# Performance work log

Hardware: AMD Instinct MI355X
Metric: run time of the kernel (lower is better)

The kernel has to match this reference:

```python
import jax, jax.numpy as jnp
import numpy as np


def setup_inputs() -> dict:
    key = jax.random.key(0)
    ks = jax.random.split(key, 13)
    B, T, C = 256, 80, 512
    H = 512
    NC = 6625
    S = 25
    s = 0.02
    inp = {
        "inputs": jax.random.normal(ks[0], (B, T, C), jnp.float32),
        "targets": jax.random.randint(ks[1], (B, S), 0, NC),
        "batch_max_length": S,
        "i2h_w": jax.random.normal(ks[2], (H, C), jnp.float32) * s,
        "h2h_w": jax.random.normal(ks[3], (H, H), jnp.float32) * s,
        "h2h_b": jax.random.normal(ks[4], (H,), jnp.float32) * s,
        "score_w": jax.random.normal(ks[5], (1, H), jnp.float32) * s,
        "gru_wih": jax.random.normal(ks[6], (3 * H, C + NC), jnp.float32) * s,
        "gru_whh": jax.random.normal(ks[7], (3 * H, H), jnp.float32) * s,
        "gru_bih": jax.random.normal(ks[8], (3 * H,), jnp.float32) * s,
        "gru_bhh": jax.random.normal(ks[9], (3 * H,), jnp.float32) * s,
        "gen_w": jax.random.normal(ks[10], (NC, H), jnp.float32) * s,
        "gen_b": jax.random.normal(ks[11], (NC,), jnp.float32) * s,
    }
    return inp


def reference(inputs, targets, batch_max_length, i2h_w, h2h_w, h2h_b, score_w,
              gru_wih, gru_whh, gru_bih, gru_bhh, gen_w, gen_b):
    B, T, C = inputs.shape
    H = h2h_w.shape[0]
    NC = gen_w.shape[0]
    S = batch_max_length

    # i2h has no bias; same result every step, hoisted out of the loop
    batch_H_proj = inputs @ i2h_w.T  # [B, T, H]
    # teacher-forcing one-hots for all steps: [S, B, NC]
    onehots = jax.nn.one_hot(targets.T, NC, dtype=inputs.dtype)

    def gru_cell(x, h):
        gi = x @ gru_wih.T + gru_bih  # [B, 3H]
        gh = h @ gru_whh.T + gru_bhh  # [B, 3H]
        i_r, i_z, i_n = jnp.split(gi, 3, axis=1)
        h_r, h_z, h_n = jnp.split(gh, 3, axis=1)
        r = jax.nn.sigmoid(i_r + h_r)
        z = jax.nn.sigmoid(i_z + h_z)
        n = jnp.tanh(i_n + r * h_n)
        return (1.0 - z) * n + z * h

    def step(h, onehot_t):
        prev_proj = h @ h2h_w.T + h2h_b  # [B, H]
        res = jnp.tanh(batch_H_proj + prev_proj[:, None, :])  # [B, T, H]
        e = jnp.einsum('bth,h->bt', res, score_w[0])  # [B, T]
        alpha = jax.nn.softmax(e, axis=1)
        context = jnp.einsum('bt,btc->bc', alpha, inputs)  # [B, C]
        x = jnp.concatenate([context, onehot_t], axis=1)  # [B, C+NC]
        h_new = gru_cell(x, h)
        return h_new, h_new

    h0 = jnp.zeros((B, H), inputs.dtype)
    _, hiddens = jax.lax.scan(step, h0, onehots)  # [S, B, H]
    output = jnp.transpose(hiddens, (1, 0, 2))  # [B, S, H]
    probs = output @ gen_w.T + gen_b  # [B, S, NC] (training path: no softmax)
    return probs
```

## Files before the change

kernel.cpp:

```cpp
#include <hip/hip_runtime.h>
#include <stdint.h>

typedef float f32x4 __attribute__((ext_vector_type(4)));
typedef int i32x4 __attribute__((ext_vector_type(4)));

#define LOG2E 1.4426950408889634f

__device__ __forceinline__ float bf2f(unsigned short u) {
  union { unsigned int i; float f; } x; x.i = ((unsigned int)u) << 16; return x.f;
}
__device__ __forceinline__ float bfu_lo(unsigned u) {
  union { unsigned int i; float f; } x; x.i = u << 16; return x.f;
}
__device__ __forceinline__ float bfu_hi(unsigned u) {
  union { unsigned int i; float f; } x; x.i = u & 0xffff0000u; return x.f;
}
__device__ __forceinline__ unsigned short f2bf(float f) {
  union { float f; unsigned int i; } x; x.f = f;
  unsigned int u = x.i + 0x7fffu + ((x.i >> 16) & 1u);
  return (unsigned short)(u >> 16);
}
__device__ __forceinline__ float fexp2(float x) {
#if __has_builtin(__builtin_amdgcn_exp2f)
  return __builtin_amdgcn_exp2f(x);
#else
  return exp2f(x);
#endif
}
__device__ __forceinline__ float frcp(float x) {
#if __has_builtin(__builtin_amdgcn_rcpf)
  return __builtin_amdgcn_rcpf(x);
#else
  return 1.f / x;
#endif
}
__device__ __forceinline__ float fast_exp(float x) { return fexp2(x * LOG2E); }
__device__ __forceinline__ float fast_tanh(float x) {
  float e = fexp2(x * (2.f * LOG2E));
  return 1.f - 2.f * frcp(e + 1.f);
}
__device__ __forceinline__ float fast_sigmoid(float x) {
  return frcp(1.f + fexp2(-x * LOG2E));
}

__device__ __forceinline__ void mfma_bf16_16x16x32(f32x4& d, i32x4 a, i32x4 b) {
  asm("v_mfma_f32_16x16x32_bf16 %0, %1, %2, %0" : "+v"(d) : "v"(a), "v"(b));
}

__device__ __forceinline__ void stage16(const unsigned short* g, unsigned short* lds_wave_base, int lane) {
#if __has_builtin(__builtin_amdgcn_global_load_lds)
  __builtin_amdgcn_global_load_lds(
      (const __attribute__((address_space(1))) unsigned int*)(uintptr_t)g,
      (__attribute__((address_space(3))) unsigned int*)(uintptr_t)lds_wave_base,
      16, 0, 0);
#else
  i32x4 v = *(const i32x4*)g;
  *(i32x4*)(lds_wave_base + lane * 8) = v;
#endif
}

__device__ __forceinline__ void xcd_swizzle(int& bx, int& by) {
  int nx = gridDim.x, nwg = nx * gridDim.y;
  if ((nwg & 7) == 0) {
    int id = by * nx + bx;
    int q = nwg >> 3;
    int swz = (id & 7) * q + (id >> 3);
    bx = swz % nx;
    by = swz / nx;
  }
}

#define BM 128
#define BN 128
#define BK 32

template <bool OUT_BF16, bool BIAS>
__device__ __forceinline__ void gemm_body(
    const unsigned short* __restrict__ A, const unsigned short* __restrict__ B,
    void* __restrict__ Cout, const float* __restrict__ bias,
    int K, int ldc, int nbound, int m0, int n0)
{
  __shared__ __align__(16) unsigned short lA[BM * BK];
  __shared__ __align__(16) unsigned short lB[BN * BK];
  const int tid = threadIdx.x;
  const int lane = tid & 63;
  const int w = tid >> 6;
  const int wm = w >> 1, wn = w & 1;
  const int frag_row = lane & 15;
  const int kgrp = lane >> 4;

  f32x4 acc[4][4];
#pragma unroll
  for (int i = 0; i < 4; ++i)
#pragma unroll
    for (int j = 0; j < 4; ++j) acc[i][j] = 0.f;

  const int nK = K / BK;
  const int c0 = tid, c1 = tid + 256;
  for (int kt = 0; kt < nK; ++kt) {
    const int kb = kt * BK;
    stage16(A + (size_t)(m0 + (c0 >> 2)) * K + kb + (c0 & 3) * 8, lA + (w * 64) * 8, lane);
    stage16(A + (size_t)(m0 + (c1 >> 2)) * K + kb + (c1 & 3) * 8, lA + (256 + w * 64) * 8, lane);
    stage16(B + (size_t)(n0 + (c0 >> 2)) * K + kb + (c0 & 3) * 8, lB + (w * 64) * 8, lane);
    stage16(B + (size_t)(n0 + (c1 >> 2)) * K + kb + (c1 & 3) * 8, lB + (256 + w * 64) * 8, lane);
    __syncthreads();

    i32x4 af[4], bfr[4];
#pragma unroll
    for (int i = 0; i < 4; ++i) {
      int ra = wm * 64 + i * 16 + frag_row;
      af[i] = *(const i32x4*)&lA[ra * BK + kgrp * 8];
      int rb = wn * 64 + i * 16 + frag_row;
      bfr[i] = *(const i32x4*)&lB[rb * BK + kgrp * 8];
    }
#pragma unroll
    for (int i = 0; i < 4; ++i)
#pragma unroll
      for (int j = 0; j < 4; ++j) mfma_bf16_16x16x32(acc[i][j], af[i], bfr[j]);
    __syncthreads();
  }

  const int crow = (lane >> 4) * 4;
  const int ccol = lane & 15;
#pragma unroll
  for (int i = 0; i < 4; ++i) {
#pragma unroll
    for (int j = 0; j < 4; ++j) {
      int gn = n0 + wn * 64 + j * 16 + ccol;
      if (gn < nbound) {
        float bv = BIAS ? bias[gn] : 0.f;
        int gmb = m0 + wm * 64 + i * 16 + crow;
#pragma unroll
        for (int r = 0; r < 4; ++r) {
          float v = acc[i][j][r] + bv;
          if (OUT_BF16) ((unsigned short*)Cout)[(size_t)(gmb + r) * ldc + gn] = f2bf(v);
          else          ((float*)Cout)[(size_t)(gmb + r) * ldc + gn] = v;
        }
      }
    }
  }
}

__global__ __launch_bounds__(256) void gemm_bf16out_kernel(
    const unsigned short* __restrict__ A, const unsigned short* __restrict__ B,
    unsigned short* __restrict__ C, int K, int ldc) {
  int bx = blockIdx.x, by = blockIdx.y;
  xcd_swizzle(bx, by);
  gemm_body<true, false>(A, B, C, nullptr, K, ldc, 1 << 30, by * BM, bx * BN);
}
__global__ __launch_bounds__(256) void gemm_f32bias_kernel(
    const unsigned short* __restrict__ A, const unsigned short* __restrict__ B,
    float* __restrict__ C, const float* __restrict__ bias, int K, int ldc, int nbound) {
  int bx = blockIdx.x, by = blockIdx.y;
  xcd_swizzle(bx, by);
  gemm_body<false, true>(A, B, C, bias, K, ldc, nbound, by * BM, bx * BN);
}

__global__ __launch_bounds__(256) void cast_bf16_kernel(
    const float* __restrict__ src, unsigned short* __restrict__ dst, int n4) {
  int i = blockIdx.x * 256 + threadIdx.x;
  if (i < n4) {
    float4 v = ((const float4*)src)[i];
    ushort4 o;
    o.x = f2bf(v.x); o.y = f2bf(v.y); o.z = f2bf(v.z); o.w = f2bf(v.w);
    ((ushort4*)dst)[i] = o;
  }
}
__global__ __launch_bounds__(256) void cast_wihc_kernel(
    const float* __restrict__ wih, unsigned short* __restrict__ dst) {
  int i = blockIdx.x * 256 + threadIdx.x;
  int j = i >> 9, c = i & 511;
  dst[i] = f2bf(wih[(size_t)j * 7137 + c]);
}
__global__ __launch_bounds__(256) void pack_h2h_kernel(
    const float* __restrict__ src, unsigned short* __restrict__ dst) {
  int i = blockIdx.x * 256 + threadIdx.x;
  int row = i >> 9, c = i & 511;
  int kb = c >> 3, kk = c & 7;
  dst[((size_t)kb * 512 + row) * 8 + kk] = f2bf(src[i]);
}
__global__ __launch_bounds__(256) void cast_genw_kernel(
    const float* __restrict__ g, unsigned short* __restrict__ dst) {
  int i = blockIdx.x * 256 + threadIdx.x;
  if (i < 6656 * 512) {
    int nrow = i >> 9, c = i & 511;
    float v = (nrow < 6625) ? g[(size_t)nrow * 512 + c] : 0.f;
    dst[i] = f2bf(v);
  }
}
__global__ __launch_bounds__(256) void transpose_oh_kernel(
    const float* __restrict__ wih, unsigned short* __restrict__ dst) {
  __shared__ float tile[32][33];
  int t0 = blockIdx.x * 32;
  int j0 = blockIdx.y * 32;
  int c = threadIdx.x & 31;
  int r4 = threadIdx.x >> 5;
#pragma unroll
  for (int rr = 0; rr < 4; ++rr) {
    int r = r4 + rr * 8;
    int tcol = t0 + c;
    tile[r][c] = (tcol < 6625) ? wih[(size_t)(j0 + r) * 7137 + 512 + tcol] : 0.f;
  }
  __syncthreads();
#pragma unroll
  for (int rr = 0; rr < 4; ++rr) {
    int r = r4 + rr * 8;
    int trow = t0 + r;
    if (trow < 6625) dst[(size_t)trow * 1536 + j0 + c] = f2bf(tile[c][r]);
  }
}

__global__ __launch_bounds__(512) void attn_step_kernel(
    const unsigned short* __restrict__ proj_bf,
    const unsigned short* __restrict__ inputs_bf,
    const unsigned short* __restrict__ h2hP,
    const float* __restrict__ h2h_b,
    const float* __restrict__ score_w,
    const unsigned short* __restrict__ h_in,
    unsigned short* __restrict__ ctx_bf,
    int s)
{
  __shared__ float h_lds[512];
  __shared__ float pp_lds[512];
  __shared__ float e_s[80];
  __shared__ float alpha_s[80];

  const int tid = threadIdx.x;
  const int lane = tid & 63;
  const int w = tid >> 6;
  const int b = blockIdx.x;

  if (s > 0) h_lds[tid] = bf2f(h_in[b * 512 + tid]);
  __syncthreads();

  float pacc = h2h_b[tid];
  if (s > 0) {
    const unsigned short* wp = h2hP + (size_t)tid * 8;
#pragma unroll 4
    for (int kb = 0; kb < 64; ++kb) {
      union { i32x4 v; unsigned int u[4]; } wu;
      wu.v = *(const i32x4*)(wp + (size_t)kb * 4096);
#pragma unroll
      for (int q = 0; q < 4; ++q) {
        pacc = fmaf(bfu_lo(wu.u[q]), h_lds[kb * 8 + 2 * q], pacc);
        pacc = fmaf(bfu_hi(wu.u[q]), h_lds[kb * 8 + 2 * q + 1], pacc);
      }
    }
  }
  pp_lds[tid] = pacc;
  __syncthreads();

  float ppv[8], swv[8];
#pragma unroll
  for (int j = 0; j < 8; ++j) ppv[j] = pp_lds[lane * 8 + j];
  *(float4*)&swv[0] = *(const float4*)(score_w + lane * 8);
  *(float4*)&swv[4] = *(const float4*)(score_w + lane * 8 + 4);

  for (int t = w; t < 80; t += 8) {
    union { i32x4 v; unsigned int u[4]; } u;
    u.v = *(const i32x4*)(proj_bf + (size_t)(b * 80 + t) * 512 + lane * 8);
    float acc = 0.f;
#pragma unroll
    for (int q = 0; q < 4; ++q) {
      acc += fast_tanh(bfu_lo(u.u[q]) + ppv[2 * q]) * swv[2 * q];
      acc += fast_tanh(bfu_hi(u.u[q]) + ppv[2 * q + 1]) * swv[2 * q + 1];
    }
#pragma unroll
    for (int m = 32; m >= 1; m >>= 1) acc += __shfl_xor(acc, m, 64);
    if (lane == 0) e_s[t] = acc;
  }
  __syncthreads();
  if (w == 0) {
    float v0 = e_s[lane];
    float v1 = (lane < 16) ? e_s[64 + lane] : -1e30f;
    float mx = fmaxf(v0, v1);
#pragma unroll
    for (int m = 32; m >= 1; m >>= 1) mx = fmaxf(mx, __shfl_xor(mx, m, 64));
    float a0 = fast_exp(v0 - mx);
    float a1 = (lane < 16) ? fast_exp(v1 - mx) : 0.f;
    float sm = a0 + a1;
#pragma unroll
    for (int m = 32; m >= 1; m >>= 1) sm += __shfl_xor(sm, m, 64);
    float inv = frcp(sm);
    alpha_s[lane] = a0 * inv;
    if (lane < 16) alpha_s[64 + lane] = a1 * inv;
  }
  __syncthreads();

  float cacc = 0.f;
  const unsigned short* ip = inputs_bf + (size_t)b * 40960;
#pragma unroll 8
  for (int t = 0; t < 80; ++t)
    cacc = fmaf(alpha_s[t], bf2f(ip[t * 512 + tid]), cacc);
  ctx_bf[(size_t)b * 512 + tid] = f2bf(cacc);
}

__global__ __launch_bounds__(256) void gru_step_kernel(
    const unsigned short* __restrict__ h_in,
    const unsigned short* __restrict__ ctx,
    const unsigned short* __restrict__ whh,
    const unsigned short* __restrict__ wihc,
    const unsigned short* __restrict__ ohT,
    const int* __restrict__ targets,
    const float* __restrict__ bih, const float* __restrict__ bhh,
    unsigned short* __restrict__ h_out,
    unsigned short* __restrict__ hid_bf,
    int s)
{
  __shared__ __align__(16) char sm[49152];
  unsigned short* lAh = (unsigned short*)sm;
  unsigned short* lAc = lAh + 4096;
  unsigned short* lBw = lAh + 8192;
  unsigned short* lBi = lAh + 14336;

  const int tid = threadIdx.x;
  const int lane = tid & 63;
  const int w = tid >> 6;
  const int fr = lane & 15, kg = lane >> 4;
  const int wm = w >> 1, wn = w & 1;
  const int m0 = blockIdx.y * 64;
  const int c0 = blockIdx.x * 32;

  f32x4 ag[2][3], ai[2][3];
#pragma unroll
  for (int i = 0; i < 2; ++i)
#pragma unroll
    for (int j = 0; j < 3; ++j) { ag[i][j] = 0.f; ai[i][j] = 0.f; }

  for (int kt = 0; kt < 8; ++kt) {
    const int kb = kt * 64;
#pragma unroll
    for (int i = 0; i < 2; ++i) {
      int c = tid + i * 256;
      int row = c >> 3, k8 = c & 7;
      int sk8 = k8 ^ (row & 7);
      stage16(h_in + (size_t)(m0 + row) * 512 + kb + sk8 * 8, lAh + (i * 256 + w * 64) * 8, lane);
      stage16(ctx  + (size_t)(m0 + row) * 512 + kb + sk8 * 8, lAc + (i * 256 + w * 64) * 8, lane);
    }
#pragma unroll
    for (int i = 0; i < 3; ++i) {
      int c = tid + i * 256;
      int br = c >> 3, k8 = c & 7;
      int sk8 = k8 ^ (br & 7);
      int gr = (br >> 5) * 512 + c0 + (br & 31);
      stage16(whh  + (size_t)gr * 512 + kb + sk8 * 8, lBw + (i * 256 + w * 64) * 8, lane);
      stage16(wihc + (size_t)gr * 512 + kb + sk8 * 8, lBi + (i * 256 + w * 64) * 8, lane);
    }
    __syncthreads();

#pragma unroll
    for (int ks = 0; ks < 2; ++ks) {
      const int kc = ks * 4 + kg;
      i32x4 ah[2], ac[2], bw[3], bi[3];
#pragma unroll
      for (int i = 0; i < 2; ++i) {
        int r = wm * 32 + i * 16 + fr;
        int off = r * 64 + (kc ^ (r & 7)) * 8;
        ah[i] = *(const i32x4*)&lAh[off];
        ac[i] = *(const i32x4*)&lAc[off];
      }
#pragma unroll
      for (int j = 0; j < 3; ++j) {
        int r = wn * 48 + j * 16 + fr;
        int off = r * 64 + (kc ^ (r & 7)) * 8;
        bw[j] = *(const i32x4*)&lBw[off];
        bi[j] = *(const i32x4*)&lBi[off];
      }
#pragma unroll
      for (int i = 0; i < 2; ++i)
#pragma unroll
        for (int j = 0; j < 3; ++j) {
          mfma_bf16_16x16x32(ag[i][j], ah[i], bw[j]);
          mfma_bf16_16x16x32(ai[i][j], ac[i], bi[j]);
        }
    }
    __syncthreads();
  }

  float* accg = (float*)sm;
  float* acci = accg + 6144;
  const int crow = (lane >> 4) * 4;
  const int ccol = lane & 15;
#pragma unroll
  for (int i = 0; i < 2; ++i)
#pragma unroll
    for (int j = 0; j < 3; ++j) {
      int col = wn * 48 + j * 16 + ccol;
#pragma unroll
      for (int r = 0; r < 4; ++r) {
        int row = wm * 32 + i * 16 + crow + r;
        accg[row * 96 + col] = ag[i][j][r];
        acci[row * 96 + col] = ai[i][j][r];
      }
    }
  __syncthreads();

#pragma unroll
  for (int e = tid; e < 2048; e += 256) {
    int row = e >> 5, cc = e & 31;
    int b = m0 + row, ch = c0 + cc;
    int tgt = targets[b * 25 + s];
    const unsigned short* oh = ohT + (size_t)tgt * 1536;
    float ghr = accg[row * 96 + cc]      + bhh[ch];
    float ghz = accg[row * 96 + 32 + cc] + bhh[512 + ch];
    float ghn = accg[row * 96 + 64 + cc] + bhh[1024 + ch];
    float gir = acci[row * 96 + cc]      + bih[ch]        + bf2f(oh[ch]);
    float giz = acci[row * 96 + 32 + cc] + bih[512 + ch]  + bf2f(oh[512 + ch]);
    float gin = acci[row * 96 + 64 + cc] + bih[1024 + ch] + bf2f(oh[1024 + ch]);
    float r_ = fast_sigmoid(gir + ghr);
    float z_ = fast_sigmoid(giz + ghz);
    float n_ = fast_tanh(gin + r_ * ghn);
    float h = (1.f - z_) * n_ + z_ * bf2f(h_in[(size_t)b * 512 + ch]);
    unsigned short hb = f2bf(h);
    h_out[(size_t)b * 512 + ch] = hb;
    hid_bf[((size_t)b * 25 + s) * 512 + ch] = hb;
  }
}

extern "C" void kernel_launch(void* const* d_in, const int* in_sizes, int n_in,
                              void* d_out, int out_size, void* d_ws, size_t ws_size,
                              hipStream_t stream) {
  (void)in_sizes; (void)n_in; (void)out_size; (void)ws_size;
  const float* inputs  = (const float*)d_in[0];
  const int*   targets = (const int*)d_in[1];
  const float* i2h_w   = (const float*)d_in[3];
  const float* h2h_w   = (const float*)d_in[4];
  const float* h2h_b   = (const float*)d_in[5];
  const float* score_w = (const float*)d_in[6];
  const float* gru_wih = (const float*)d_in[7];
  const float* gru_whh = (const float*)d_in[8];
  const float* gru_bih = (const float*)d_in[9];
  const float* gru_bhh = (const float*)d_in[10];
  const float* gen_w   = (const float*)d_in[11];
  const float* gen_b   = (const float*)d_in[12];
  float* out = (float*)d_out;

  char* ws = (char*)d_ws;
  size_t off = 0;
  auto alloc = [&](size_t bytes) {
    char* p = ws + off;
    off += (bytes + 255) & ~(size_t)255;
    return p;
  };
  unsigned short* inputs_bf = (unsigned short*)alloc(10485760ull * 2);
  unsigned short* proj_bf   = (unsigned short*)alloc(10485760ull * 2);
  unsigned short* i2h_bf    = (unsigned short*)alloc(262144ull * 2);
  unsigned short* h2hP_bf   = (unsigned short*)alloc(262144ull * 2);
  unsigned short* whh_bf    = (unsigned short*)alloc(786432ull * 2);
  unsigned short* wihc_bf   = (unsigned short*)alloc(786432ull * 2);
  unsigned short* ohT_bf    = (unsigned short*)alloc(10176000ull * 2);
  unsigned short* genw_bf   = (unsigned short*)alloc(3407872ull * 2);
  unsigned short* ctx_bf    = (unsigned short*)alloc(131072ull * 2);
  unsigned short* hbuf0     = (unsigned short*)alloc(131072ull * 2);
  unsigned short* hbuf1     = (unsigned short*)alloc(131072ull * 2);
  unsigned short* hid_bf    = (unsigned short*)alloc(3276800ull * 2);

  cast_bf16_kernel<<<10240, 256, 0, stream>>>(inputs, inputs_bf, 2621440);
  cast_bf16_kernel<<<256, 256, 0, stream>>>(i2h_w, i2h_bf, 65536);
  pack_h2h_kernel<<<1024, 256, 0, stream>>>(h2h_w, h2hP_bf);
  cast_bf16_kernel<<<768, 256, 0, stream>>>(gru_whh, whh_bf, 196608);
  cast_wihc_kernel<<<3072, 256, 0, stream>>>(gru_wih, wihc_bf);
  transpose_oh_kernel<<<dim3(208, 48), 256, 0, stream>>>(gru_wih, ohT_bf);
  cast_genw_kernel<<<13312, 256, 0, stream>>>(gen_w, genw_bf);
  gemm_bf16out_kernel<<<dim3(4, 160), 256, 0, stream>>>(inputs_bf, i2h_bf, proj_bf, 512, 512);
  hipMemsetAsync(hbuf0, 0, 131072 * 2, stream);

  unsigned short* hb[2] = {hbuf0, hbuf1};
  for (int s = 0; s < 25; ++s) {
    attn_step_kernel<<<256, 512, 0, stream>>>(
        proj_bf, inputs_bf, h2hP_bf, h2h_b, score_w, hb[s & 1], ctx_bf, s);
    gru_step_kernel<<<dim3(16, 4), 256, 0, stream>>>(
        hb[s & 1], ctx_bf, whh_bf, wihc_bf, ohT_bf, targets,
        gru_bih, gru_bhh, hb[(s + 1) & 1], hid_bf, s);
  }

  gemm_f32bias_kernel<<<dim3(52, 50), 256, 0, stream>>>(hid_bf, genw_bf, out, gen_b, 512, 6625, 6625);
}
```

Before: 975.4 us.

## Fuse per-step attention and GRU kernels into one persistent cooperative kernel

Replaces the 50 separate launches (attention plus GRU for each of 25 steps) with a single cooperative persistent kernel. Blocks move between phases through a two-level atomic grid barrier, and h and ctx pass between phases as relaxed agent-scope atomic loads and stores. The GRU phase now runs on 128 blocks with 32-row tiles, and the previous hidden state is kept in registers instead of being re-read. This is meant to remove launch overhead and inter-kernel gaps. The cost is spin-barrier latency, half the blocks sitting idle during the GRU phase, and 90KB of LDS per block limiting residency.

```diff
diff --git a/kernel.cpp b/kernel.cpp
--- a/kernel.cpp
+++ b/kernel.cpp
@@ -57,6 +57,13 @@
   i32x4 v = *(const i32x4*)g;
   *(i32x4*)(lds_wave_base + lane * 8) = v;
 #endif
+}
+
+__device__ __forceinline__ void st_u64_dc(void* p, unsigned long long v) {
+  __hip_atomic_store((unsigned long long*)p, v, __ATOMIC_RELAXED, __HIP_MEMORY_SCOPE_AGENT);
+}
+__device__ __forceinline__ unsigned long long ld_u64_dc(const void* p) {
+  return __hip_atomic_load((unsigned long long*)p, __ATOMIC_RELAXED, __HIP_MEMORY_SCOPE_AGENT);
 }
 
 __device__ __forceinline__ void xcd_swizzle(int& bx, int& by) {
@@ -210,210 +217,252 @@
   }
 }
 
-__global__ __launch_bounds__(512) void attn_step_kernel(
+__device__ __forceinline__ void gbar(unsigned* bar, int bid, unsigned it) {
+  asm volatile("s_waitcnt vmcnt(0) lgkmcnt(0)" ::: "memory");
+  __syncthreads();
+  if (threadIdx.x == 0) {
+    unsigned* leaf = bar + (bid >> 5) * 32;
+    unsigned* root = bar + 512;
+    unsigned* gate = bar + 544;
+    unsigned p = __hip_atomic_fetch_add(leaf, 1u, __ATOMIC_RELAXED, __HIP_MEMORY_SCOPE_AGENT);
+    if (p == it * 32u - 1u) {
+      unsigned q = __hip_atomic_fetch_add(root, 1u, __ATOMIC_RELAXED, __HIP_MEMORY_SCOPE_AGENT);
+      if (q == it * 8u - 1u)
+        __hip_atomic_store(gate, it, __ATOMIC_RELAXED, __HIP_MEMORY_SCOPE_AGENT);
+    }
+    while (__hip_atomic_load(gate, __ATOMIC_RELAXED, __HIP_MEMORY_SCOPE_AGENT) < it)
+      __builtin_amdgcn_s_sleep(1);
+  }
+  __syncthreads();
+}
+
+__global__ __launch_bounds__(512) void loop_kernel(
     const unsigned short* __restrict__ proj_bf,
     const unsigned short* __restrict__ inputs_bf,
     const unsigned short* __restrict__ h2hP,
     const float* __restrict__ h2h_b,
     const float* __restrict__ score_w,
-    const unsigned short* __restrict__ h_in,
-    unsigned short* __restrict__ ctx_bf,
-    int s)
-{
-  __shared__ float h_lds[512];
-  __shared__ float pp_lds[512];
-  __shared__ float e_s[80];
-  __shared__ float alpha_s[80];
-
-  const int tid = threadIdx.x;
-  const int lane = tid & 63;
-  const int w = tid >> 6;
-  const int b = blockIdx.x;
-
-  if (s > 0) h_lds[tid] = bf2f(h_in[b * 512 + tid]);
-  __syncthreads();
-
-  float pacc = h2h_b[tid];
-  if (s > 0) {
-    const unsigned short* wp = h2hP + (size_t)tid * 8;
-#pragma unroll 4
-    for (int kb = 0; kb < 64; ++kb) {
-      union { i32x4 v; unsigned int u[4]; } wu;
-      wu.v = *(const i32x4*)(wp + (size_t)kb * 4096);
-#pragma unroll
-      for (int q = 0; q < 4; ++q) {
-        pacc = fmaf(bfu_lo(wu.u[q]), h_lds[kb * 8 + 2 * q], pacc);
-        pacc = fmaf(bfu_hi(wu.u[q]), h_lds[kb * 8 + 2 * q + 1], pacc);
-      }
-    }
-  }
-  pp_lds[tid] = pacc;
-  __syncthreads();
-
-  float ppv[8], swv[8];
-#pragma unroll
-  for (int j = 0; j < 8; ++j) ppv[j] = pp_lds[lane * 8 + j];
-  *(float4*)&swv[0] = *(const float4*)(score_w + lane * 8);
-  *(float4*)&swv[4] = *(const float4*)(score_w + lane * 8 + 4);
-
-  for (int t = w; t < 80; t += 8) {
-    union { i32x4 v; unsigned int u[4]; } u;
-    u.v = *(const i32x4*)(proj_bf + (size_t)(b * 80 + t) * 512 + lane * 8);
-    float acc = 0.f;
-#pragma unroll
-    for (int q = 0; q < 4; ++q) {
-      acc += fast_tanh(bfu_lo(u.u[q]) + ppv[2 * q]) * swv[2 * q];
-      acc += fast_tanh(bfu_hi(u.u[q]) + ppv[2 * q + 1]) * swv[2 * q + 1];
-    }
-#pragma unroll
-    for (int m = 32; m >= 1; m >>= 1) acc += __shfl_xor(acc, m, 64);
-    if (lane == 0) e_s[t] = acc;
-  }
-  __syncthreads();
-  if (w == 0) {
-    float v0 = e_s[lane];
-    float v1 = (lane < 16) ? e_s[64 + lane] : -1e30f;
-    float mx = fmaxf(v0, v1);
-#pragma unroll
-    for (int m = 32; m >= 1; m >>= 1) mx = fmaxf(mx, __shfl_xor(mx, m, 64));
-    float a0 = fast_exp(v0 - mx);
-    float a1 = (lane < 16) ? fast_exp(v1 - mx) : 0.f;
-    float sm = a0 + a1;
-#pragma unroll
-    for (int m = 32; m >= 1; m >>= 1) sm += __shfl_xor(sm, m, 64);
-    float inv = frcp(sm);
-    alpha_s[lane] = a0 * inv;
-    if (lane < 16) alpha_s[64 + lane] = a1 * inv;
-  }
-  __syncthreads();
-
-  float cacc = 0.f;
-  const unsigned short* ip = inputs_bf + (size_t)b * 40960;
-#pragma unroll 8
-  for (int t = 0; t < 80; ++t)
-    cacc = fmaf(alpha_s[t], bf2f(ip[t * 512 + tid]), cacc);
-  ctx_bf[(size_t)b * 512 + tid] = f2bf(cacc);
-}
-
-__global__ __launch_bounds__(256) void gru_step_kernel(
-    const unsigned short* __restrict__ h_in,
-    const unsigned short* __restrict__ ctx,
     const unsigned short* __restrict__ whh,
     const unsigned short* __restrict__ wihc,
     const unsigned short* __restrict__ ohT,
     const int* __restrict__ targets,
     const float* __restrict__ bih, const float* __restrict__ bhh,
-    unsigned short* __restrict__ h_out,
+    unsigned short* __restrict__ ctx_bf,
+    unsigned short* __restrict__ h_bf,
     unsigned short* __restrict__ hid_bf,
-    int s)
+    unsigned* bar)
 {
-  __shared__ __align__(16) char sm[49152];
-  unsigned short* lAh = (unsigned short*)sm;
-  unsigned short* lAc = lAh + 4096;
-  unsigned short* lBw = lAh + 8192;
-  unsigned short* lBi = lAh + 14336;
+  extern __shared__ char smem[];
+  unsigned short* lAh   = (unsigned short*)smem;
+  unsigned short* lActx = (unsigned short*)(smem + 32768);
+  unsigned short* lBw   = (unsigned short*)(smem + 65536);
+  unsigned short* lBi   = (unsigned short*)(smem + 77824);
+  float* accg = (float*)(smem + 65536);
+  float* acci = (float*)(smem + 77824);
+  unsigned short* hpk = (unsigned short*)(smem + 90112);
+  float* h_lds   = (float*)smem;
+  float* pp_lds  = (float*)(smem + 2048);
+  float* e_s     = (float*)(smem + 4096);
+  float* alpha_s = (float*)(smem + 4416);
+  unsigned short* cpk = (unsigned short*)(smem + 4736);
 
   const int tid = threadIdx.x;
   const int lane = tid & 63;
   const int w = tid >> 6;
+  const int bid = blockIdx.x;
+  const int b = bid;
   const int fr = lane & 15, kg = lane >> 4;
-  const int wm = w >> 1, wn = w & 1;
-  const int m0 = blockIdx.y * 64;
-  const int c0 = blockIdx.x * 32;
-
-  f32x4 ag[2][3], ai[2][3];
-#pragma unroll
-  for (int i = 0; i < 2; ++i)
-#pragma unroll
-    for (int j = 0; j < 3; ++j) { ag[i][j] = 0.f; ai[i][j] = 0.f; }
-
-  for (int kt = 0; kt < 8; ++kt) {
-    const int kb = kt * 64;
-#pragma unroll
-    for (int i = 0; i < 2; ++i) {
-      int c = tid + i * 256;
-      int row = c >> 3, k8 = c & 7;
-      int sk8 = k8 ^ (row & 7);
-      stage16(h_in + (size_t)(m0 + row) * 512 + kb + sk8 * 8, lAh + (i * 256 + w * 64) * 8, lane);
-      stage16(ctx  + (size_t)(m0 + row) * 512 + kb + sk8 * 8, lAc + (i * 256 + w * 64) * 8, lane);
+  const int bx = bid & 15, by = bid >> 4;
+  const int m0 = by * 32, c0ch = bx * 32;
+
+  float swv[8];
+  *(float4*)&swv[0] = *(const float4*)(score_w + lane * 8);
+  *(float4*)&swv[4] = *(const float4*)(score_w + lane * 8 + 4);
+
+  float h_old0 = 0.f, h_old1 = 0.f;
+  unsigned it = 0;
+  __syncthreads();
+
+  for (int s = 0; s < 25; ++s) {
+    {
+      if (s > 0 && tid < 128) {
+        unsigned long long v = ld_u64_dc(h_bf + (size_t)b * 512 + tid * 4);
+        h_lds[tid * 4 + 0] = bf2f((unsigned short)(v));
+        h_lds[tid * 4 + 1] = bf2f((unsigned short)(v >> 16));
+        h_lds[tid * 4 + 2] = bf2f((unsigned short)(v >> 32));
+        h_lds[tid * 4 + 3] = bf2f((unsigned short)(v >> 48));
+      }
+      __syncthreads();
+      float pacc = h2h_b[tid];
+      if (s > 0) {
+        const unsigned short* wp = h2hP + (size_t)tid * 8;
+#pragma unroll 4
+        for (int kb = 0; kb < 64; ++kb) {
+          union { i32x4 v; unsigned int u[4]; } wu;
+          wu.v = *(const i32x4*)(wp + (size_t)kb * 4096);
+#pragma unroll
+          for (int q = 0; q < 4; ++q) {
+            pacc = fmaf(bfu_lo(wu.u[q]), h_lds[kb * 8 + 2 * q], pacc);
+            pacc = fmaf(bfu_hi(wu.u[q]), h_lds[kb * 8 + 2 * q + 1], pacc);
+          }
+        }
+      }
+      pp_lds[tid] = pacc;
+      __syncthreads();
+
+      float ppv[8];
+#pragma unroll
+      for (int j = 0; j < 8; ++j) ppv[j] = pp_lds[lane * 8 + j];
+
+      for (int t = w; t < 80; t += 8) {
+        union { i32x4 v; unsigned int u[4]; } u;
+        u.v = *(const i32x4*)(proj_bf + (size_t)(b * 80 + t) * 512 + lane * 8);
+        float acc = 0.f;
+#pragma unroll
+        for (int q = 0; q < 4; ++q) {
+          acc += fast_tanh(bfu_lo(u.u[q]) + ppv[2 * q]) * swv[2 * q];
+          acc += fast_tanh(bfu_hi(u.u[q]) + ppv[2 * q + 1]) * swv[2 * q + 1];
+        }
+#pragma unroll
+        for (int m = 32; m >= 1; m >>= 1) acc += __shfl_xor(acc, m, 64);
+        if (lane == 0) e_s[t] = acc;
+      }
+      __syncthreads();
+      if (w == 0) {
+        float v0 = e_s[lane];
+        float v1 = (lane < 16) ? e_s[64 + lane] : -1e30f;
+        float mx = fmaxf(v0, v1);
+#pragma unroll
+        for (int m = 32; m >= 1; m >>= 1) mx = fmaxf(mx, __shfl_xor(mx, m, 64));
+        float a0 = fast_exp(v0 - mx);
+        float a1 = (lane < 16) ? fast_exp(v1 - mx) : 0.f;
+        float sm = a0 + a1;
+#pragma unroll
+        for (int m = 32; m >= 1; m >>= 1) sm += __shfl_xor(sm, m, 64);
+        float inv = frcp(sm);
+        alpha_s[lane] = a0 * inv;
+        if (lane < 16) alpha_s[64 + lane] = a1 * inv;
+      }
+      __syncthreads();
+      float cacc = 0.f;
+      const unsigned short* ip = inputs_bf + (size_t)b * 40960;
+#pragma unroll 8
+      for (int t = 0; t < 80; ++t)
+        cacc = fmaf(alpha_s[t], bf2f(ip[t * 512 + tid]), cacc);
+      cpk[tid] = f2bf(cacc);
+      __syncthreads();
+      if (tid < 128)
+        st_u64_dc(&ctx_bf[(size_t)b * 512 + tid * 4], *(const unsigned long long*)(cpk + tid * 4));
     }
-#pragma unroll
-    for (int i = 0; i < 3; ++i) {
-      int c = tid + i * 256;
-      int br = c >> 3, k8 = c & 7;
-      int sk8 = k8 ^ (br & 7);
-      int gr = (br >> 5) * 512 + c0 + (br & 31);
-      stage16(whh  + (size_t)gr * 512 + kb + sk8 * 8, lBw + (i * 256 + w * 64) * 8, lane);
-      stage16(wihc + (size_t)gr * 512 + kb + sk8 * 8, lBi + (i * 256 + w * 64) * 8, lane);
+    ++it; gbar(bar, bid, it);
+
+    if (bid < 128) {
+#pragma unroll
+      for (int i = 0; i < 8; ++i) {
+        int c = tid + i * 512;
+        int row = c >> 7;
+        int q = c & 127, ch = q >> 1, pc = q & 1;
+        int dst = row * 512 + (ch ^ (row & 7)) * 8 + pc * 4;
+        size_t src = (size_t)(m0 + row) * 512 + ch * 8 + pc * 4;
+        *(unsigned long long*)(lAh + dst) = ld_u64_dc(h_bf + src);
+        *(unsigned long long*)(lActx + dst) = ld_u64_dc(ctx_bf + src);
+      }
+
+      f32x4 ag[3], ai[3];
+#pragma unroll
+      for (int j = 0; j < 3; ++j) { ag[j] = 0.f; ai[j] = 0.f; }
+      const int wm = w >> 1, wn = w & 1;
+
+      for (int kt = 0; kt < 8; ++kt) {
+        const int kb = kt * 64;
+        {
+          int br = tid >> 3, k8 = tid & 7, sk8 = k8 ^ (br & 7);
+          int gr = (br >> 5) * 512 + c0ch + (br & 31);
+          stage16(whh  + (size_t)gr * 512 + kb + sk8 * 8, lBw + (w * 64) * 8, lane);
+          stage16(wihc + (size_t)gr * 512 + kb + sk8 * 8, lBi + (w * 64) * 8, lane);
+          if (w < 4) {
+            int c2 = 512 + tid;
+            int br2 = c2 >> 3, k82 = c2 & 7, sk82 = k82 ^ (br2 & 7);
+            int gr2 = (br2 >> 5) * 512 + c0ch + (br2 & 31);
+            stage16(whh  + (size_t)gr2 * 512 + kb + sk82 * 8, lBw + (512 + w * 64) * 8, lane);
+            stage16(wihc + (size_t)gr2 * 512 + kb + sk82 * 8, lBi + (512 + w * 64) * 8, lane);
+          }
+        }
+        __syncthreads();
+        if (w < 4) {
+#pragma unroll
+          for (int ks = 0; ks < 2; ++ks) {
+            const int ckA = kt * 8 + ks * 4 + kg;
+            const int rA = wm * 16 + fr;
+            const int aoff = rA * 512 + (ckA ^ (rA & 7)) * 8;
+            i32x4 a_h = *(const i32x4*)&lAh[aoff];
+            i32x4 a_c = *(const i32x4*)&lActx[aoff];
+            const int kc = ks * 4 + kg;
+            i32x4 bw[3], bi[3];
+#pragma unroll
+            for (int j = 0; j < 3; ++j) {
+              int rB = wn * 48 + j * 16 + fr;
+              int off = rB * 64 + (kc ^ (rB & 7)) * 8;
+              bw[j] = *(const i32x4*)&lBw[off];
+              bi[j] = *(const i32x4*)&lBi[off];
+            }
+#pragma unroll
+            for (int j = 0; j < 3; ++j) {
+              mfma_bf16_16x16x32(ag[j], a_h, bw[j]);
+              mfma_bf16_16x16x32(ai[j], a_c, bi[j]);
+            }
+          }
+        }
+        __syncthreads();
+      }
+
+      if (w < 4) {
+        const int crow = (lane >> 4) * 4;
+        const int ccol = lane & 15;
+#pragma unroll
+        for (int j = 0; j < 3; ++j) {
+          int col = wn * 48 + j * 16 + ccol;
+#pragma unroll
+          for (int r = 0; r < 4; ++r) {
+            int row = wm * 16 + crow + r;
+            accg[row * 96 + col] = ag[j][r];
+            acci[row * 96 + col] = ai[j][r];
+          }
+        }
+      }
+      __syncthreads();
+
+#pragma unroll
+      for (int half = 0; half < 2; ++half) {
+        int e = tid + half * 512;
+        int row = e >> 5, cc = e & 31;
+        int b_ = m0 + row, ch = c0ch + cc;
+        int tgt = targets[b_ * 25 + s];
+        const unsigned short* oh = ohT + (size_t)tgt * 1536;
+        float ghr = accg[row * 96 + cc]      + bhh[ch];
+        float ghz = accg[row * 96 + 32 + cc] + bhh[512 + ch];
+        float ghn = accg[row * 96 + 64 + cc] + bhh[1024 + ch];
+        float gir = acci[row * 96 + cc]      + bih[ch]        + bf2f(oh[ch]);
+        float giz = acci[row * 96 + 32 + cc] + bih[512 + ch]  + bf2f(oh[512 + ch]);
+        float gin = acci[row * 96 + 64 + cc] + bih[1024 + ch] + bf2f(oh[1024 + ch]);
+        float r_ = fast_sigmoid(gir + ghr);
+        float z_ = fast_sigmoid(giz + ghz);
+        float n_ = fast_tanh(gin + r_ * ghn);
+        float hprev = half ? h_old1 : h_old0;
+        float h = (1.f - z_) * n_ + z_ * hprev;
+        if (half) h_old1 = h; else h_old0 = h;
+        unsigned short hb = f2bf(h);
+        hid_bf[((size_t)b_ * 25 + s) * 512 + ch] = hb;
+        hpk[row * 32 + cc] = hb;
+      }
+      __syncthreads();
+      if (tid < 256) {
+        int row = tid >> 3, c4 = (tid & 7) * 4;
+        st_u64_dc(&h_bf[(size_t)(m0 + row) * 512 + c0ch + c4],
+                  *(const unsigned long long*)(hpk + row * 32 + c4));
+      }
     }
-    __syncthreads();
-
-#pragma unroll
-    for (int ks = 0; ks < 2; ++ks) {
-      const int kc = ks * 4 + kg;
-      i32x4 ah[2], ac[2], bw[3], bi[3];
-#pragma unroll
-      for (int i = 0; i < 2; ++i) {
-        int r = wm * 32 + i * 16 + fr;
-        int off = r * 64 + (kc ^ (r & 7)) * 8;
-        ah[i] = *(const i32x4*)&lAh[off];
-        ac[i] = *(const i32x4*)&lAc[off];
-      }
-#pragma unroll
-      for (int j = 0; j < 3; ++j) {
-        int r = wn * 48 + j * 16 + fr;
-        int off = r * 64 + (kc ^ (r & 7)) * 8;
-        bw[j] = *(const i32x4*)&lBw[off];
-        bi[j] = *(const i32x4*)&lBi[off];
-      }
-#pragma unroll
-      for (int i = 0; i < 2; ++i)
-#pragma unroll
-        for (int j = 0; j < 3; ++j) {
-          mfma_bf16_16x16x32(ag[i][j], ah[i], bw[j]);
-          mfma_bf16_16x16x32(ai[i][j], ac[i], bi[j]);
-        }
-    }
-    __syncthreads();
-  }
-
-  float* accg = (float*)sm;
-  float* acci = accg + 6144;
-  const int crow = (lane >> 4) * 4;
-  const int ccol = lane & 15;
-#pragma unroll
-  for (int i = 0; i < 2; ++i)
-#pragma unroll
-    for (int j = 0; j < 3; ++j) {
-      int col = wn * 48 + j * 16 + ccol;
-#pragma unroll
-      for (int r = 0; r < 4; ++r) {
-        int row = wm * 32 + i * 16 + crow + r;
-        accg[row * 96 + col] = ag[i][j][r];
-        acci[row * 96 + col] = ai[i][j][r];
-      }
-    }
-  __syncthreads();
-
-#pragma unroll
-  for (int e = tid; e < 2048; e += 256) {
-    int row = e >> 5, cc = e & 31;
-    int b = m0 + row, ch = c0 + cc;
-    int tgt = targets[b * 25 + s];
-    const unsigned short* oh = ohT + (size_t)tgt * 1536;
-    float ghr = accg[row * 96 + cc]      + bhh[ch];
-    float ghz = accg[row * 96 + 32 + cc] + bhh[512 + ch];
-    float ghn = accg[row * 96 + 64 + cc] + bhh[1024 + ch];
-    float gir = acci[row * 96 + cc]      + bih[ch]        + bf2f(oh[ch]);
-    float giz = acci[row * 96 + 32 + cc] + bih[512 + ch]  + bf2f(oh[512 + ch]);
-    float gin = acci[row * 96 + 64 + cc] + bih[1024 + ch] + bf2f(oh[1024 + ch]);
-    float r_ = fast_sigmoid(gir + ghr);
-    float z_ = fast_sigmoid(giz + ghz);
-    float n_ = fast_tanh(gin + r_ * ghn);
-    float h = (1.f - z_) * n_ + z_ * bf2f(h_in[(size_t)b * 512 + ch]);
-    unsigned short hb = f2bf(h);
-    h_out[(size_t)b * 512 + ch] = hb;
-    hid_bf[((size_t)b * 25 + s) * 512 + ch] = hb;
+    ++it; gbar(bar, bid, it);
   }
 }
 
@@ -451,9 +500,9 @@
   unsigned short* ohT_bf    = (unsigned short*)alloc(10176000ull * 2);
   unsigned short* genw_bf   = (unsigned short*)alloc(3407872ull * 2);
   unsigned short* ctx_bf    = (unsigned short*)alloc(131072ull * 2);
-  unsigned short* hbuf0     = (unsigned short*)alloc(131072ull * 2);
-  unsigned short* hbuf1     = (unsigned short*)alloc(131072ull * 2);
+  unsigned short* h_bf      = (unsigned short*)alloc(131072ull * 2);
   unsigned short* hid_bf    = (unsigned short*)alloc(3276800ull * 2);
+  unsigned*       bar       = (unsigned*)alloc(1024ull * 4);
 
   cast_bf16_kernel<<<10240, 256, 0, stream>>>(inputs, inputs_bf, 2621440);
   cast_bf16_kernel<<<256, 256, 0, stream>>>(i2h_w, i2h_bf, 65536);
@@ -463,15 +512,18 @@
   transpose_oh_kernel<<<dim3(208, 48), 256, 0, stream>>>(gru_wih, ohT_bf);
   cast_genw_kernel<<<13312, 256, 0, stream>>>(gen_w, genw_bf);
   gemm_bf16out_kernel<<<dim3(4, 160), 256, 0, stream>>>(inputs_bf, i2h_bf, proj_bf, 512, 512);
-  hipMemsetAsync(hbuf0, 0, 131072 * 2, stream);
-
-  unsigned short* hb[2] = {hbuf0, hbuf1};
-  for (int s = 0; s < 25; ++s) {
-    attn_step_kernel<<<256, 512, 0, stream>>>(
-        proj_bf, inputs_bf, h2hP_bf, h2h_b, score_w, hb[s & 1], ctx_bf, s);
-    gru_step_kernel<<<dim3(16, 4), 256, 0, stream>>>(
-        hb[s & 1], ctx_bf, whh_bf, wihc_bf, ohT_bf, targets,
-        gru_bih, gru_bhh, hb[(s + 1) & 1], hid_bf, s);
+  hipMemsetAsync(h_bf, 0, 131072 * 2, stream);
+  hipMemsetAsync(bar, 0, 4096, stream);
+
+  {
+    void* args[] = {
+      (void*)&proj_bf, (void*)&inputs_bf, (void*)&h2hP_bf, (void*)&h2h_b,
+      (void*)&score_w, (void*)&whh_bf, (void*)&wihc_bf, (void*)&ohT_bf,
+      (void*)&targets, (void*)&gru_bih, (void*)&gru_bhh,
+      (void*)&ctx_bf, (void*)&h_bf, (void*)&hid_bf, (void*)&bar
+    };
+    hipLaunchCooperativeKernel(reinterpret_cast<void*>(loop_kernel),
+                               dim3(256), dim3(512), args, 92160, stream);
   }
 
   gemm_f32bias_kernel<<<dim3(52, 50), 256, 0, stream>>>(hid_bf, genw_bf, out, gen_b, 512, 6625, 6625);
```

Result: slower. 1.547 ms (+58.6%).
